# Kernel optimization log

Measured on AMD Instinct MI355X. Metric: run time of the kernel, lower is better.

Reference implementation:

```python
import jax, jax.numpy as jnp
import numpy as np

IN, HID, OUT, HEADS = 64, 128, 256, 4
BL, N, E = 4, 2500, 120000
NT = BL * N  # total flattened nodes = 10000
NEG_SLOPE = 0.2  # PyG GATv2Conv default


def setup_inputs() -> dict:
    key = jax.random.key(0)
    ks = jax.random.split(key, 32)
    inp = {}
    inp["x"] = jax.random.normal(ks[0], (BL, N, IN), jnp.float32)
    inp["edge_index"] = jax.random.randint(ks[1], (2, E), 0, NT, jnp.int32)
    inp["edge_weight"] = jax.random.uniform(ks[2], (E, 1), jnp.float32)
    # layers: (fan_in, out_per_head, heads)
    dims = [(IN, HID, HEADS), (HID * HEADS, HID, HEADS), (HID * HEADS, OUT, 1)]
    i = 3
    for l, (fi, fo, h) in enumerate(dims):
        sc = 1.0 / np.sqrt(fi)
        inp[f"Wl{l}"] = jax.random.normal(ks[i], (fi, h * fo), jnp.float32) * sc
        inp[f"bl{l}"] = jax.random.normal(ks[i + 1], (h * fo,), jnp.float32) * 0.01
        inp[f"Wr{l}"] = jax.random.normal(ks[i + 2], (fi, h * fo), jnp.float32) * sc
        inp[f"br{l}"] = jax.random.normal(ks[i + 3], (h * fo,), jnp.float32) * 0.01
        inp[f"We{l}"] = jax.random.normal(ks[i + 4], (1, h * fo), jnp.float32)
        inp[f"att{l}"] = jax.random.normal(ks[i + 5], (h, fo), jnp.float32) / np.sqrt(fo)
        inp[f"bias{l}"] = jax.random.normal(ks[i + 6], (h * fo,), jnp.float32) * 0.01
        i += 7
    return inp


def _gat_layer(x, src, dst, ew, Wl, bl, Wr, br, We, att, bias):
    # x: (NT, F); ew: (E, 1); att: (H, C)
    H, C = att.shape
    n = x.shape[0]
    xl = (x @ Wl + bl).reshape(n, H, C)          # source transform
    xr = (x @ Wr + br).reshape(n, H, C)          # target transform
    xe = (ew @ We).reshape(-1, H, C)             # edge-attr transform (no bias in PyG lin_edge)
    e = jax.nn.leaky_relu(xl[src] + xr[dst] + xe, negative_slope=NEG_SLOPE)  # (E, H, C)
    logits = jnp.einsum('ehc,hc->eh', e, att)    # (E, H)
    # segment softmax over incoming edges of each destination node
    m = jax.lax.stop_gradient(jax.ops.segment_max(logits, dst, num_segments=n))
    m = jnp.where(jnp.isfinite(m), m, 0.0)
    p = jnp.exp(logits - m[dst])
    s = jax.ops.segment_sum(p, dst, num_segments=n)
    alpha = p / (s[dst] + 1e-16)                 # (E, H)
    msg = xl[src] * alpha[:, :, None]            # (E, H, C)
    out = jax.ops.segment_sum(msg, dst, num_segments=n)  # (NT, H, C)
    return out.reshape(n, H * C) + bias


def reference(x, edge_index, edge_weight,
              Wl0, bl0, Wr0, br0, We0, att0, bias0,
              Wl1, bl1, Wr1, br1, We1, att1, bias1,
              Wl2, bl2, Wr2, br2, We2, att2, bias2):
    bl_, n_, f_ = x.shape
    h = x.reshape(bl_ * n_, f_)
    src, dst = edge_index[0], edge_index[1]
    h = jax.nn.elu(_gat_layer(h, src, dst, edge_weight, Wl0, bl0, Wr0, br0, We0, att0, bias0))
    h = jax.nn.elu(_gat_layer(h, src, dst, edge_weight, Wl1, bl1, Wr1, br1, We1, att1, bias1))
    h = _gat_layer(h, src, dst, edge_weight, Wl2, bl2, Wr2, br2, We2, att2, bias2)
    return h.reshape(bl_, n_, -1)
```

## Files before the change

kernel.cpp:

```cpp
#include <hip/hip_runtime.h>
#include <hip/hip_bf16.h>
#include <math.h>

#define NT    10000
#define NE    120000
#define MP    10240

using h8    = __attribute__((ext_vector_type(8))) _Float16;
using h4    = __attribute__((ext_vector_type(4))) _Float16;
using f32x4 = __attribute__((ext_vector_type(4))) float;

struct Args {
    const float* x;
    const int*   src;
    const int*   dst;
    const float* ew;
    const float* W[6];
    const float* bl[3];
    const float* br[3];
    const float* We[3];
    const float* att[3];
    const float* bias[3];
    _Float16* wt[6];
    _Float16* xf;
    _Float16* xl;  _Float16* xr;
    _Float16* af;
    float* out;
    int* rowptr; int* cntcur; int* csr_src; float* csr_w;
};

__device__ __forceinline__ void gemm_jobs(
    const _Float16* __restrict__ A,
    const _Float16* __restrict__ WlT, const _Float16* __restrict__ WrT,
    const float* __restrict__ biasl, const float* __restrict__ biasr,
    _Float16* __restrict__ outl, _Float16* __restrict__ outr,
    int M, int N, int K, int njobs, int job0, int jstep, _Float16* sm)
{
    _Float16* sA = sm;
    _Float16* sB = sm + 8192;

    int tid = threadIdx.x;
    int wave = tid >> 6, lane = tid & 63;
    int lr15 = lane & 15;
    int lk8  = (lane >> 4) * 8;
    int fq = lane >> 4;
    int fc = lane & 15;
    int wm = (wave & 1) << 6;
    int wn = (wave >> 1) << 6;

    for (int job = job0; job < njobs; job += jstep) {
        int xcd = job & 7;
        int kk  = job >> 3;
        int r   = kk % 10;
        int byy = kk / 10;
        int bm  = (xcd * 10 + r) * 128;

        int nby = N >> 7;
        bool isR = byy >= nby;
        int bnn = (isR ? byy - nby : byy) << 7;
        const _Float16* Bh = isR ? WrT : WlT;
        const float* bias  = isR ? biasr : biasl;
        _Float16* out      = isR ? outr : outl;

        f32x4 acc[4][4] = {};

        for (int k0 = 0; k0 < K; k0 += 64) {
            __syncthreads();
            #pragma unroll
            for (int q = 0; q < 8; ++q) {
                int p = wave * 8 + q;
                int bufi = p >> 4;
                int c = p & 15;
                int sub = c >> 3, rg = c & 7;
                const _Float16* g = (bufi == 0) ? A : Bh;
                int rowbase = (bufi == 0) ? bm : bnn;
                _Float16* sb = sm + bufi * 8192 + c * 512;
                const _Float16* gp = g + (size_t)(rowbase + rg * 16 + lr15) * K
                                       + k0 + sub * 32 + lk8;
                __builtin_amdgcn_global_load_lds(
                    (const __attribute__((address_space(1))) void*)gp,
                    (__attribute__((address_space(3))) void*)sb,
                    16, 0, 0);
            }
            __syncthreads();

            #pragma unroll
            for (int sub = 0; sub < 2; ++sub) {
                h8 af[4];
                #pragma unroll
                for (int i = 0; i < 4; ++i) {
                    int c = sub * 8 + (wave & 1) * 4 + i;
                    af[i] = *(const h8*)(sA + c * 512 + lane * 8);
                }
                #pragma unroll
                for (int j = 0; j < 4; ++j) {
                    int c = sub * 8 + (wave >> 1) * 4 + j;
                    h8 bf = *(const h8*)(sB + c * 512 + lane * 8);
                    #pragma unroll
                    for (int i = 0; i < 4; ++i)
                        acc[i][j] = __builtin_amdgcn_mfma_f32_16x16x32_f16(af[i], bf, acc[i][j], 0, 0, 0);
                }
            }
        }

        #pragma unroll
        for (int j = 0; j < 4; ++j) {
            int col = bnn + wn + j * 16 + fc;
            float bv = bias[col];
            #pragma unroll
            for (int i = 0; i < 4; ++i) {
                int row0 = bm + wm + i * 16 + fq * 4;
                #pragma unroll
                for (int reg = 0; reg < 4; ++reg) {
                    int row = row0 + reg;
                    if (row < M)
                        out[(size_t)row * N + col] = (_Float16)(acc[i][j][reg] + bv);
                }
            }
        }
    }
}

__global__ void preph_k(Args a) {
    __shared__ float sf[32 * 33];
    const int mat_cum[7] = {0, 32, 64, 320, 576, 704, 832};
    const int mat_K[6]   = {64, 64, 512, 512, 512, 512};
    const int mat_N[6]   = {512, 512, 512, 512, 256, 256};
    int tid = threadIdx.x;
    int tx = tid & 31, ty = tid >> 5;
    for (int w = blockIdx.x; w < 3332; w += gridDim.x) {
        if (w < 832) {
            int t = w;
            int mm = 0;
            #pragma unroll
            for (int q = 1; q < 6; ++q) if (t >= mat_cum[q]) mm = q;
            int tt = t - mat_cum[mm];
            int K = mat_K[mm], N = mat_N[mm];
            int tiles_k = K >> 5;
            int tk = tt % tiles_k, tn = tt / tiles_k;
            const float* W = a.W[mm];
            _Float16* T = a.wt[mm];
            int bk = tk * 32, bn = tn * 32;
            __syncthreads();
            #pragma unroll
            for (int i = 0; i < 4; ++i)
                sf[(ty * 4 + i) * 33 + tx] =
                    W[(size_t)(bk + ty * 4 + i) * N + bn + tx];
            __syncthreads();
            #pragma unroll
            for (int i = 0; i < 4; ++i) {
                int nn = ty * 4 + i;
                T[(size_t)(bn + nn) * K + bk + tx] = (_Float16)sf[tx * 33 + nn];
            }
        } else {
            int i = (w - 832) * 256 + tid;
            a.xf[i] = (_Float16)a.x[i];
        }
    }
    for (int e = blockIdx.x * 256 + tid; e < NE; e += gridDim.x * 256)
        atomicAdd(&a.cntcur[a.dst[e]], 1);
}

__global__ __launch_bounds__(1024) void scan_k(Args a) {
    __shared__ int si[1024];
    int tid = threadIdx.x;
    const int PER = 10;
    int base = tid * PER;
    int s = 0;
    for (int i = 0; i < PER; ++i) {
        int idx = base + i;
        if (idx < NT) s += a.cntcur[idx];
    }
    si[tid] = s;
    __syncthreads();
    for (int off = 1; off < 1024; off <<= 1) {
        int v = (tid >= off) ? si[tid - off] : 0;
        __syncthreads();
        si[tid] += v;
        __syncthreads();
    }
    int run = (tid == 0) ? 0 : si[tid - 1];
    for (int i = 0; i < PER; ++i) {
        int idx = base + i;
        if (idx < NT) { a.rowptr[idx] = run; run += a.cntcur[idx]; }
        else if (idx == NT) a.rowptr[idx] = run;
    }
}

__global__ __launch_bounds__(256, 4) void scatgemm_k(Args a) {
    __shared__ __align__(16) _Float16 sm[2 * 8192];
    int b = blockIdx.x;
    if (b < 160) {
        int* cursor = a.cntcur + NT;
        for (int e = b * 256 + (int)threadIdx.x; e < NE; e += 160 * 256) {
            int d = a.dst[e];
            int pos = atomicAdd(&cursor[d], 1);
            int idx = a.rowptr[d] + pos;
            a.csr_src[idx] = a.src[e];
            a.csr_w[idx]  = a.ew[e];
        }
    } else {
        gemm_jobs(a.xf, a.wt[0], a.wt[1], a.bl[0], a.br[0],
                  a.xl, a.xr, NT, 512, 64, 640, b - 160, 640, sm);
    }
}

__global__ __launch_bounds__(256, 4) void gemm_k(
    const _Float16* A, const _Float16* WlT, const _Float16* WrT,
    const float* bl, const float* br,
    _Float16* ol, _Float16* orr, int M, int N, int K, int njobs) {
    __shared__ __align__(16) _Float16 sm[2 * 8192];
    gemm_jobs(A, WlT, WrT, bl, br, ol, orr, M, N, K, njobs,
              blockIdx.x, gridDim.x, sm);
}

template<int C, int H, bool DO_ELU, bool FP16OUT>
__global__ __launch_bounds__(256) void edge_k(
    const _Float16* __restrict__ xl, const _Float16* __restrict__ xr,
    const int* __restrict__ rowptr, const int* __restrict__ csr_src,
    const float* __restrict__ csr_w,
    const float* __restrict__ We, const float* __restrict__ att,
    const float* __restrict__ bias,
    float* __restrict__ outf, _Float16* __restrict__ outh)
{
    constexpr int CHT = C * H;
    constexpr int VPT = CHT / 64;
    constexpr int G   = 64 / H;

    int node = (blockIdx.x * 256 + threadIdx.x) >> 6;
    int lane = threadIdx.x & 63;
    if (node >= NT) return;
    int c0 = lane * VPT;
    size_t nbase = (size_t)node * CHT + c0;

    float xr_reg[VPT], we_reg[VPT], att_reg[VPT], bias_reg[VPT];
    {
        _Float16 t[VPT];
        if (VPT == 8) *(h8*)t = *(const h8*)(xr + nbase);
        else          *(h4*)t = *(const h4*)(xr + nbase);
        #pragma unroll
        for (int v = 0; v < VPT; ++v) xr_reg[v] = (float)t[v];
    }
    #pragma unroll
    for (int v = 0; v < VPT; v += 4) {
        *(float4*)(we_reg + v)   = *(const float4*)(We + c0 + v);
        *(float4*)(att_reg + v)  = *(const float4*)(att + c0 + v);
        *(float4*)(bias_reg + v) = *(const float4*)(bias + c0 + v);
    }

    int rs = rowptr[node];
    int re = rowptr[node + 1];

    float m = -INFINITY, ssum = 0.f;
    float av[VPT];
    #pragma unroll
    for (int v = 0; v < VPT; ++v) av[v] = 0.f;

    for (int base = rs; base < re; base += 64) {
        int cn = re - base;
        if (cn > 64) cn = 64;
        int le = base + lane;
        int cl = (le < re) ? le : (re - 1);
        int   sidx = csr_src[cl];
        float swt  = csr_w[cl];

        _Float16 r0[VPT], r1[VPT], r2[VPT], r3[VPT];
        auto ld = [&](int j, _Float16* dst) {
            int s = __shfl(sidx, j, 64);
            const _Float16* p = xl + (size_t)s * CHT + c0;
            if (VPT == 8) *(h8*)dst = *(const h8*)p;
            else          *(h4*)dst = *(const h4*)p;
        };
        auto step = [&](const _Float16* rc, int j) {
            float w = __shfl(swt, j, 64);
            float xlv[VPT];
            #pragma unroll
            for (int v = 0; v < VPT; ++v) xlv[v] = (float)rc[v];
            float part = 0.f;
            #pragma unroll
            for (int v = 0; v < VPT; ++v) {
                float t = xlv[v] + xr_reg[v] + w * we_reg[v];
                t = fmaxf(t, 0.f) + 0.2f * fminf(t, 0.f);
                part += t * att_reg[v];
            }
            #pragma unroll
            for (int off = G / 2; off > 0; off >>= 1)
                part += __shfl_xor(part, off, 64);
            float newm = fmaxf(m, part);
            float fac = __expf(m - newm);
            float p = __expf(part - newm);
            ssum = ssum * fac + p;
            #pragma unroll
            for (int v = 0; v < VPT; ++v) av[v] = av[v] * fac + p * xlv[v];
            m = newm;
        };

        ld(0, r0);
        if (cn > 1) ld(1, r1);
        if (cn > 2) ld(2, r2);
        if (cn > 3) ld(3, r3);

        int j = 0;
        while (j < cn) {
            step(r0, j);
            if (j + 4 < cn) ld(j + 4, r0);
            if (++j >= cn) break;
            step(r1, j);
            if (j + 4 < cn) ld(j + 4, r1);
            if (++j >= cn) break;
            step(r2, j);
            if (j + 4 < cn) ld(j + 4, r2);
            if (++j >= cn) break;
            step(r3, j);
            if (j + 4 < cn) ld(j + 4, r3);
            ++j;
        }
    }

    float inv = 1.f / (ssum + 1e-16f);
    #pragma unroll
    for (int v = 0; v < VPT; ++v) {
        float o = av[v] * inv + bias_reg[v];
        if (DO_ELU) o = (o > 0.f) ? o : (__expf(o) - 1.f);
        if (FP16OUT) outh[nbase + v] = (_Float16)o;
        else         outf[nbase + v] = o;
    }
}

extern "C" void kernel_launch(void* const* d_in, const int* in_sizes, int n_in,
                              void* d_out, int out_size, void* d_ws, size_t ws_size,
                              hipStream_t stream) {
    Args a;
    a.x   = (const float*)d_in[0];
    const int* ei = (const int*)d_in[1];
    a.src = ei;
    a.dst = ei + NE;
    a.ew  = (const float*)d_in[2];
    for (int l = 0; l < 3; ++l) {
        int base = 3 + 7 * l;
        a.W[2 * l]     = (const float*)d_in[base + 0];
        a.bl[l]        = (const float*)d_in[base + 1];
        a.W[2 * l + 1] = (const float*)d_in[base + 2];
        a.br[l]        = (const float*)d_in[base + 3];
        a.We[l]        = (const float*)d_in[base + 4];
        a.att[l]       = (const float*)d_in[base + 5];
        a.bias[l]      = (const float*)d_in[base + 6];
    }

    size_t off = 0;
    auto alloc = [&](size_t bytes) -> void* {
        void* p = (char*)d_ws + off;
        off += (bytes + 255) & ~(size_t)255;
        return p;
    };
    a.xl   = (_Float16*)alloc((size_t)MP * 512 * 2);
    a.xr   = (_Float16*)alloc((size_t)MP * 512 * 2);
    a.af   = (_Float16*)alloc((size_t)MP * 512 * 2);
    a.xf   = (_Float16*)alloc((size_t)MP * 64 * 2);
    const int KD[3] = {64, 512, 512};
    const int ND[3] = {512, 512, 256};
    for (int l = 0; l < 3; ++l) {
        a.wt[2 * l]     = (_Float16*)alloc((size_t)KD[l] * ND[l] * 2);
        a.wt[2 * l + 1] = (_Float16*)alloc((size_t)KD[l] * ND[l] * 2);
    }
    a.rowptr  = (int*)alloc((size_t)(NT + 1) * 4);
    a.cntcur  = (int*)alloc((size_t)2 * NT * 4);
    a.csr_src = (int*)alloc((size_t)NE * 4);
    a.csr_w   = (float*)alloc((size_t)NE * 4);
    a.out     = (float*)d_out;

    hipMemsetAsync(a.cntcur, 0, (size_t)2 * NT * 4, stream);
    preph_k<<<640, 256, 0, stream>>>(a);
    scan_k<<<1, 1024, 0, stream>>>(a);
    scatgemm_k<<<800, 256, 0, stream>>>(a);

    edge_k<128, 4, true, true><<<2500, 256, 0, stream>>>(
        a.xl, a.xr, a.rowptr, a.csr_src, a.csr_w,
        a.We[0], a.att[0], a.bias[0], nullptr, a.af);

    gemm_k<<<640, 256, 0, stream>>>(a.af, a.wt[2], a.wt[3],
                                    a.bl[1], a.br[1], a.xl, a.xr,
                                    NT, 512, 512, 640);
    edge_k<128, 4, true, true><<<2500, 256, 0, stream>>>(
        a.xl, a.xr, a.rowptr, a.csr_src, a.csr_w,
        a.We[1], a.att[1], a.bias[1], nullptr, a.af);

    gemm_k<<<320, 256, 0, stream>>>(a.af, a.wt[4], a.wt[5],
                                    a.bl[2], a.br[2], a.xl, a.xr,
                                    NT, 256, 512, 320);
    edge_k<256, 1, false, false><<<2500, 256, 0, stream>>>(
        a.xl, a.xr, a.rowptr, a.csr_src, a.csr_w,
        a.We[2], a.att[2], a.bias[2], a.out, nullptr);
}
```

Before: 283.4 us.

## Fold scan into preph via last-block pattern, deepen edge prefetch, skip rescale

The separate single-block scan kernel is removed. The last block to finish preph_k, found through an atomic counter, now does the prefix scan into rowptr using shared memory. The edge kernel's gather prefetch depth grows from 4 to 6 rows, and a wave-uniform fast path skips the online-softmax rescale when no lane's new logit exceeds the running max. In exchange, preph_k uses about 40KB more LDS, which may lower its occupancy. The scan also now runs at the tail of preph_k on a single block with 256 threads instead of 1024.

Result: slower. 354.7 us (+25.2%).

```diff
diff --git a/kernel.cpp b/kernel.cpp
--- a/kernel.cpp
+++ b/kernel.cpp
@@ -123,6 +123,9 @@
 
 __global__ void preph_k(Args a) {
     __shared__ float sf[32 * 33];
+    __shared__ int   sp[256];
+    __shared__ int   scnt[10240];
+    __shared__ int   sdone;
     const int mat_cum[7] = {0, 32, 64, 320, 576, 704, 832};
     const int mat_K[6]   = {64, 64, 512, 512, 512, 512};
     const int mat_N[6]   = {512, 512, 512, 512, 256, 256};
@@ -159,30 +162,36 @@
     }
     for (int e = blockIdx.x * 256 + tid; e < NE; e += gridDim.x * 256)
         atomicAdd(&a.cntcur[a.dst[e]], 1);
-}
-
-__global__ __launch_bounds__(1024) void scan_k(Args a) {
-    __shared__ int si[1024];
-    int tid = threadIdx.x;
-    const int PER = 10;
-    int base = tid * PER;
+
+    __threadfence();
+    if (tid == 0) sdone = atomicAdd(&a.cntcur[2 * NT], 1);
+    __syncthreads();
+    if (sdone != (int)gridDim.x - 1) return;
+    __threadfence();
+    const int PER = 40;
+    int b0 = tid * PER;
     int s = 0;
     for (int i = 0; i < PER; ++i) {
-        int idx = base + i;
-        if (idx < NT) s += a.cntcur[idx];
-    }
-    si[tid] = s;
+        int idx = b0 + i;
+        int v = 0;
+        if (idx < NT)
+            v = __hip_atomic_load(&a.cntcur[idx], __ATOMIC_RELAXED,
+                                  __HIP_MEMORY_SCOPE_AGENT);
+        scnt[idx] = v;
+        s += v;
+    }
+    sp[tid] = s;
     __syncthreads();
-    for (int off = 1; off < 1024; off <<= 1) {
-        int v = (tid >= off) ? si[tid - off] : 0;
+    for (int off = 1; off < 256; off <<= 1) {
+        int v2 = (tid >= off) ? sp[tid - off] : 0;
         __syncthreads();
-        si[tid] += v;
+        sp[tid] += v2;
         __syncthreads();
     }
-    int run = (tid == 0) ? 0 : si[tid - 1];
+    int run = (tid == 0) ? 0 : sp[tid - 1];
     for (int i = 0; i < PER; ++i) {
-        int idx = base + i;
-        if (idx < NT) { a.rowptr[idx] = run; run += a.cntcur[idx]; }
+        int idx = b0 + i;
+        if (idx < NT) { a.rowptr[idx] = run; run += scnt[idx]; }
         else if (idx == NT) a.rowptr[idx] = run;
     }
 }
@@ -264,7 +273,7 @@
         int   sidx = csr_src[cl];
         float swt  = csr_w[cl];
 
-        _Float16 r0[VPT], r1[VPT], r2[VPT], r3[VPT];
+        _Float16 r0[VPT], r1[VPT], r2[VPT], r3[VPT], r4[VPT], r5[VPT];
         auto ld = [&](int j, _Float16* dst) {
             int s = __shfl(sidx, j, 64);
             const _Float16* p = xl + (size_t)s * CHT + c0;
@@ -286,33 +295,48 @@
             #pragma unroll
             for (int off = G / 2; off > 0; off >>= 1)
                 part += __shfl_xor(part, off, 64);
-            float newm = fmaxf(m, part);
-            float fac = __expf(m - newm);
-            float p = __expf(part - newm);
-            ssum = ssum * fac + p;
-            #pragma unroll
-            for (int v = 0; v < VPT; ++v) av[v] = av[v] * fac + p * xlv[v];
-            m = newm;
+            if (__all(part <= m)) {
+                float p = __expf(part - m);
+                ssum += p;
+                #pragma unroll
+                for (int v = 0; v < VPT; ++v) av[v] += p * xlv[v];
+            } else {
+                float newm = fmaxf(m, part);
+                float fac = __expf(m - newm);
+                float p = __expf(part - newm);
+                ssum = ssum * fac + p;
+                #pragma unroll
+                for (int v = 0; v < VPT; ++v) av[v] = av[v] * fac + p * xlv[v];
+                m = newm;
+            }
         };
 
         ld(0, r0);
         if (cn > 1) ld(1, r1);
         if (cn > 2) ld(2, r2);
         if (cn > 3) ld(3, r3);
+        if (cn > 4) ld(4, r4);
+        if (cn > 5) ld(5, r5);
 
         int j = 0;
         while (j < cn) {
             step(r0, j);
-            if (j + 4 < cn) ld(j + 4, r0);
+            if (j + 6 < cn) ld(j + 6, r0);
             if (++j >= cn) break;
             step(r1, j);
-            if (j + 4 < cn) ld(j + 4, r1);
+            if (j + 6 < cn) ld(j + 6, r1);
             if (++j >= cn) break;
             step(r2, j);
-            if (j + 4 < cn) ld(j + 4, r2);
+            if (j + 6 < cn) ld(j + 6, r2);
             if (++j >= cn) break;
             step(r3, j);
-            if (j + 4 < cn) ld(j + 4, r3);
+            if (j + 6 < cn) ld(j + 6, r3);
+            if (++j >= cn) break;
+            step(r4, j);
+            if (j + 6 < cn) ld(j + 6, r4);
+            if (++j >= cn) break;
+            step(r5, j);
+            if (j + 6 < cn) ld(j + 6, r5);
             ++j;
         }
     }
@@ -364,14 +388,13 @@
         a.wt[2 * l + 1] = (_Float16*)alloc((size_t)KD[l] * ND[l] * 2);
     }
     a.rowptr  = (int*)alloc((size_t)(NT + 1) * 4);
-    a.cntcur  = (int*)alloc((size_t)2 * NT * 4);
+    a.cntcur  = (int*)alloc((size_t)(2 * NT + 4) * 4);
     a.csr_src = (int*)alloc((size_t)NE * 4);
     a.csr_w   = (float*)alloc((size_t)NE * 4);
     a.out     = (float*)d_out;
 
-    hipMemsetAsync(a.cntcur, 0, (size_t)2 * NT * 4, stream);
+    hipMemsetAsync(a.cntcur, 0, (size_t)(2 * NT + 4) * 4, stream);
     preph_k<<<640, 256, 0, stream>>>(a);
-    scan_k<<<1, 1024, 0, stream>>>(a);
     scatgemm_k<<<800, 256, 0, stream>>>(a);
 
     edge_k<128, 4, true, true><<<2500, 256, 0, stream>>>(
```
